# Kernel optimization log

Hardware: AMD Instinct MI355X
Metric: run time of the kernel (lower is better)

Reference implementation:

```python
import jax, jax.numpy as jnp
import numpy as np

NH, NKV, HD = 16, 4, 64  # num_heads, num_kv_heads, head_dim
ROPE_BASE = 10000.0


def setup_inputs() -> dict:
    key = jax.random.key(0)
    ks = jax.random.split(key, 5)
    B, S, D = 2, 2048, 1024
    x = jax.random.normal(ks[0], (B, S, D), dtype=jnp.float32)
    # torch Linear layout: [out_features, in_features], xavier-ish scale
    Wq = jax.random.normal(ks[1], (NH * HD, D), dtype=jnp.float32) * 0.02
    Wk = jax.random.normal(ks[2], (NKV * HD, D), dtype=jnp.float32) * 0.02
    Wv = jax.random.normal(ks[3], (NKV * HD, D), dtype=jnp.float32) * 0.02
    Wo = jax.random.normal(ks[4], (D, NH * HD), dtype=jnp.float32) * 0.02
    return {"x": x, "Wq": Wq, "Wk": Wk, "Wv": Wv, "Wo": Wo}


def _rotate_half(t):
    t1, t2 = jnp.split(t, 2, axis=-1)
    return jnp.concatenate([-t2, t1], axis=-1)


def _rope_cos_sin(seq_len, dtype):
    inv_freq = 1.0 / (ROPE_BASE ** (jnp.arange(0, HD, 2, dtype=jnp.float32) / HD))
    freqs = jnp.outer(jnp.arange(seq_len, dtype=jnp.float32), inv_freq)  # [S, HD/2]
    emb = jnp.concatenate([freqs, freqs], axis=-1)                       # [S, HD]
    return jnp.cos(emb).astype(dtype), jnp.sin(emb).astype(dtype)


def reference(x, Wq, Wk, Wv, Wo):
    B, S, D = x.shape
    scale = 1.0 / np.sqrt(HD)
    # projections (torch Linear: y = x @ W.T)
    q = jnp.einsum('bsd,ed->bse', x, Wq).reshape(B, S, NH, HD).transpose(0, 2, 1, 3)
    k = jnp.einsum('bsd,ed->bse', x, Wk).reshape(B, S, NKV, HD).transpose(0, 2, 1, 3)
    v = jnp.einsum('bsd,ed->bse', x, Wv).reshape(B, S, NKV, HD).transpose(0, 2, 1, 3)
    # RoPE
    cos, sin = _rope_cos_sin(S, x.dtype)
    cos = cos[None, None]  # [1,1,S,HD]
    sin = sin[None, None]
    q = q * cos + _rotate_half(q) * sin
    k = k * cos + _rotate_half(k) * sin
    # GQA: repeat kv heads (matches expand+reshape: head h = kvh*rep + r)
    rep = NH // NKV
    k = jnp.repeat(k, rep, axis=1)  # [B,NH,S,HD]
    v = jnp.repeat(v, rep, axis=1)
    # scaled dot-product attention, causal
    scores = jnp.einsum('bhqd,bhkd->bhqk', q, k) * scale
    causal = jnp.triu(jnp.ones((S, S), dtype=bool), k=1)
    scores = jnp.where(causal, jnp.float32(-jnp.inf), scores)
    attn = jax.nn.softmax(scores.astype(jnp.float32), axis=-1).astype(q.dtype)
    out = jnp.einsum('bhqk,bhkd->bhqd', attn, v)
    out = out.transpose(0, 2, 1, 3).reshape(B, S, NH * HD)
    return jnp.einsum('bse,de->bsd', out, Wo)
```

## Files before the change

### kernel.cpp

```cpp
#include <hip/hip_runtime.h>
#include <hip/hip_bf16.h>
#include <math.h>

#define B_    2
#define S_    2048
#define D_    1024
#define NH_   16
#define NKV_  4
#define HD_   64
#define NTOK  (B_ * S_)
#define QKVN  (NH_ * HD_ + 2 * NKV_ * HD_)
#define REP   (NH_ / NKV_)

#define LOG2E 1.4426950408889634f

typedef __attribute__((ext_vector_type(8))) short short8;
typedef __attribute__((ext_vector_type(4))) float f32x4;

__device__ short  g_xb[(size_t)NTOK * D_];
__device__ short  g_wqkv[(size_t)QKVN * D_];
__device__ short  g_wob[(size_t)D_ * NH_ * HD_];
__device__ float  g_rc[(size_t)S_ * 32];
__device__ float  g_rs[(size_t)S_ * 32];
__device__ short  g_qb[(size_t)B_ * NH_  * S_ * HD_];
__device__ short  g_kb[(size_t)B_ * NKV_ * S_ * HD_];
__device__ short  g_vt[(size_t)B_ * NKV_ * HD_ * S_];
__device__ short  g_ao[(size_t)NTOK * NH_ * HD_];

static __device__ inline short f2bf(float f) {
  __hip_bfloat16 h = __float2bfloat16(f);
  return *reinterpret_cast<short*>(&h);
}
static __device__ inline unsigned pack2(float lo, float hi) {
  return ((unsigned)(unsigned short)f2bf(hi) << 16) | (unsigned)(unsigned short)f2bf(lo);
}

#define NX4   (NTOK * D_ / 4)
#define NWQ4  (NH_ * HD_ * D_ / 4)
#define NWK4  (NKV_ * HD_ * D_ / 4)
#define NWV4  NWK4
#define NWO4  (D_ * NH_ * HD_ / 4)
#define NCVT  (NX4 + NWQ4 + NWK4 + NWV4 + NWO4)

__global__ __launch_bounds__(256) void convert_all(const float* __restrict__ x,
                                                   const float* __restrict__ wq,
                                                   const float* __restrict__ wk,
                                                   const float* __restrict__ wv,
                                                   const float* __restrict__ wo) {
  int i = blockIdx.x * blockDim.x + threadIdx.x;
  if (i >= NCVT) return;
  const float* src; short* dst; int off;
  if (i < NX4)                          { src = x;  dst = g_xb;   off = i; }
  else if (i < NX4 + NWQ4)              { src = wq; dst = g_wqkv; off = i - NX4; }
  else if (i < NX4 + NWQ4 + NWK4)       { src = wk; dst = g_wqkv + (size_t)NWQ4 * 4;          off = i - NX4 - NWQ4; }
  else if (i < NX4 + NWQ4 + NWK4 + NWV4){ src = wv; dst = g_wqkv + (size_t)(NWQ4 + NWK4) * 4; off = i - NX4 - NWQ4 - NWK4; }
  else                                  { src = wo; dst = g_wob;  off = i - NX4 - NWQ4 - NWK4 - NWV4; }
  float4 v = ((const float4*)src)[off];
  short4 s;
  s.x = f2bf(v.x); s.y = f2bf(v.y); s.z = f2bf(v.z); s.w = f2bf(v.w);
  ((short4*)dst)[off] = s;
}

__global__ __launch_bounds__(256) void rope_tbl() {
  int i = blockIdx.x * blockDim.x + threadIdx.x;
  if (i >= S_ * 32) return;
  const int d = i & 31, s = i >> 5;
  const float inv = exp2f((float)d * (-13.287712379549449f / 32.0f));
  const float ang = (float)s * inv;
  float sn, cs;
  sincosf(ang, &sn, &cs);
  g_rc[i] = cs; g_rs[i] = sn;
}

__global__ __launch_bounds__(256) void gemm_qkv_rope() {
  const int w = threadIdx.x >> 6, lane = threadIdx.x & 63;
  const int m0 = blockIdx.x * 128 + w * 32;
  const int nb = blockIdx.y;
  const int n0 = nb * 64;
  const int lr = lane & 15, lk = (lane >> 4) * 8;

  f32x4 acc[2][4] = {};
  for (int k0 = 0; k0 < D_; k0 += 32) {
    short8 a0 = *(const short8*)(g_xb + (size_t)(m0 + lr) * D_ + k0 + lk);
    short8 a1 = *(const short8*)(g_xb + (size_t)(m0 + 16 + lr) * D_ + k0 + lk);
#pragma unroll
    for (int bj = 0; bj < 4; ++bj) {
      short8 bf = *(const short8*)(g_wqkv + (size_t)(n0 + bj * 16 + lr) * D_ + k0 + lk);
      acc[0][bj] = __builtin_amdgcn_mfma_f32_16x16x32_bf16(a0, bf, acc[0][bj], 0, 0, 0);
      acc[1][bj] = __builtin_amdgcn_mfma_f32_16x16x32_bf16(a1, bf, acc[1][bj], 0, 0, 0);
    }
  }
  const int rb = (lane >> 4) * 4;

  if (nb < 20) {
    const float sc = (nb < 16) ? 0.125f * LOG2E : 1.0f;
    short* const base = (nb < 16) ? g_qb : g_kb;
    const int hh = (nb < 16) ? nb : (nb - 16);
    const int nhh = (nb < 16) ? NH_ : NKV_;
#pragma unroll
    for (int af = 0; af < 2; ++af)
#pragma unroll
      for (int bj = 0; bj < 2; ++bj) {
        const int d0 = bj * 16 + lr;
#pragma unroll
        for (int r = 0; r < 4; ++r) {
          const int tok = m0 + af * 16 + rb + r;
          const int bI = tok >> 11, s = tok & (S_ - 1);
          const float c  = g_rc[s * 32 + d0];
          const float sn = g_rs[s * 32 + d0];
          const float lo = acc[af][bj][r], hi = acc[af][bj + 2][r];
          short* dp = base + (((size_t)(bI * nhh + hh)) * S_ + s) * HD_;
          dp[d0]      = f2bf((lo * c - hi * sn) * sc);
          dp[d0 + 32] = f2bf((hi * c + lo * sn) * sc);
        }
      }
  } else {
    const int kvh = nb - 20;
#pragma unroll
    for (int af = 0; af < 2; ++af)
#pragma unroll
      for (int bj = 0; bj < 4; ++bj) {
        const int d = bj * 16 + lr;
        const int tok0 = m0 + af * 16 + rb;
        const int bI = tok0 >> 11, s0 = tok0 & (S_ - 1);
        short4 s4;
        s4.x = f2bf(acc[af][bj][0]); s4.y = f2bf(acc[af][bj][1]);
        s4.z = f2bf(acc[af][bj][2]); s4.w = f2bf(acc[af][bj][3]);
        *(short4*)(g_vt + (((size_t)(bI * NKV_ + kvh)) * HD_ + d) * S_ + s0) = s4;
      }
  }
}

__global__ __launch_bounds__(256) void attn_mfma() {
  const int bh  = blockIdx.x;
  const int b   = bh >> 4, h = bh & 15;
  const int kvh = h >> 2;
  const int qw  = (int)(gridDim.y - 1 - blockIdx.y);
  const int w   = threadIdx.x >> 6;
  const int lane = threadIdx.x & 63;
  const int g = lane >> 4, l = lane & 15;
  const int q0 = qw * 16;
  const int q_glob = q0 + l;

  const short* Qb = g_qb + ((size_t)bh * S_ + q0) * HD_;
  const short* Kb = g_kb + ((size_t)(b * NKV_ + kvh)) * S_ * HD_;
  const short* Vt = g_vt + ((size_t)(b * NKV_ + kvh)) * HD_ * S_;

  short8 qf[2];
  qf[0] = *(const short8*)(Qb + l * HD_ + g * 8);
  qf[1] = *(const short8*)(Qb + l * HD_ + 32 + g * 8);

  f32x4 o[4] = {};
  float m_run = -1e30f, l_part = 0.0f;

  const int nt = (q0 >> 5) + 1;
  for (int t = w; t < nt; t += 4) {
    const short* Kt = Kb + (size_t)(t * 32) * HD_;
    short8 kf0 = *(const short8*)(Kt + l * HD_ + g * 8);
    short8 kf1 = *(const short8*)(Kt + (16 + l) * HD_ + g * 8);
    short8 kf2 = *(const short8*)(Kt + l * HD_ + 32 + g * 8);
    short8 kf3 = *(const short8*)(Kt + (16 + l) * HD_ + 32 + g * 8);
    short8 vf[4];
#pragma unroll
    for (int df = 0; df < 4; ++df)
      vf[df] = *(const short8*)(Vt + (size_t)(df * 16 + l) * S_ + t * 32 + g * 8);

    f32x4 st[2] = {};
    st[0] = __builtin_amdgcn_mfma_f32_16x16x32_bf16(kf0, qf[0], st[0], 0, 0, 0);
    st[1] = __builtin_amdgcn_mfma_f32_16x16x32_bf16(kf1, qf[0], st[1], 0, 0, 0);
    st[0] = __builtin_amdgcn_mfma_f32_16x16x32_bf16(kf2, qf[1], st[0], 0, 0, 0);
    st[1] = __builtin_amdgcn_mfma_f32_16x16x32_bf16(kf3, qf[1], st[1], 0, 0, 0);

    float sv[2][4];
    float mt = -1e30f;
#pragma unroll
    for (int mf = 0; mf < 2; ++mf)
#pragma unroll
      for (int r = 0; r < 4; ++r) {
        const int kv = t * 32 + mf * 16 + g * 4 + r;
        float s = st[mf][r];
        s = (kv > q_glob) ? -1e30f : s;
        sv[mf][r] = s;
        mt = fmaxf(mt, s);
      }
    if (__any(mt > m_run + 8.0f)) {
      float mr = mt;
      mr = fmaxf(mr, __shfl_xor(mr, 16, 64));
      mr = fmaxf(mr, __shfl_xor(mr, 32, 64));
      const float m_new = fmaxf(m_run, mr);
      const float alpha = exp2f(m_run - m_new);
      l_part *= alpha;
#pragma unroll
      for (int df = 0; df < 4; ++df)
#pragma unroll
        for (int r = 0; r < 4; ++r) o[df][r] *= alpha;
      m_run = m_new;
    }
    float p[2][4];
#pragma unroll
    for (int mf = 0; mf < 2; ++mf)
#pragma unroll
      for (int r = 0; r < 4; ++r) {
        const float pv = exp2f(sv[mf][r] - m_run);
        p[mf][r] = pv;
        l_part += pv;
      }
    unsigned u0 = pack2(p[0][0], p[0][1]);
    unsigned u1 = pack2(p[0][2], p[0][3]);
    unsigned u2 = pack2(p[1][0], p[1][1]);
    unsigned u3 = pack2(p[1][2], p[1][3]);
    const int srcA = ((g & 1) << 5) + l;
    const int srcB = srcA + 16;
    const unsigned a0 = __shfl(u0, srcA, 64), a2 = __shfl(u2, srcA, 64);
    const unsigned b1 = __shfl(u1, srcA, 64), b3 = __shfl(u3, srcA, 64);
    const unsigned c0 = __shfl(u0, srcB, 64), c2 = __shfl(u2, srcB, 64);
    const unsigned d1 = __shfl(u1, srcB, 64), d3 = __shfl(u3, srcB, 64);
    const bool hi = (g & 2);
    unsigned W[4];
    W[0] = hi ? a2 : a0;  W[1] = hi ? b3 : b1;
    W[2] = hi ? c2 : c0;  W[3] = hi ? d3 : d1;
    short8 pt = *reinterpret_cast<short8*>(W);

#pragma unroll
    for (int df = 0; df < 4; ++df)
      o[df] = __builtin_amdgcn_mfma_f32_16x16x32_bf16(vf[df], pt, o[df], 0, 0, 0);
  }

  float l1 = l_part + __shfl_xor(l_part, 16, 64);
  const float l_tot = l1 + __shfl_xor(l1, 32, 64);

  __shared__ float lds_m[4][16];
  __shared__ float lds_l[4][16];
  __shared__ float lds_o[4][16][68];
  if (g == 0) { lds_m[w][l] = m_run; lds_l[w][l] = l_tot; }
#pragma unroll
  for (int df = 0; df < 4; ++df)
#pragma unroll
    for (int r = 0; r < 4; ++r)
      lds_o[w][l][df * 16 + g * 4 + r] = o[df][r];
  __syncthreads();

  const int tid = threadIdx.x;
  const int q = tid & 15, dg = tid >> 4;
  float ms = lds_m[0][q];
#pragma unroll
  for (int w2 = 1; w2 < 4; ++w2) ms = fmaxf(ms, lds_m[w2][q]);
  float lsum = 0.0f;
  float od[4] = {0.0f, 0.0f, 0.0f, 0.0f};
#pragma unroll
  for (int w2 = 0; w2 < 4; ++w2) {
    const float sc = exp2f(lds_m[w2][q] - ms);
    lsum += lds_l[w2][q] * sc;
#pragma unroll
    for (int j = 0; j < 4; ++j) od[j] += sc * lds_o[w2][q][dg * 4 + j];
  }
  const float inv_l = 1.0f / lsum;
  short* optr = g_ao + ((size_t)(b * S_ + q0 + q)) * (NH_ * HD_) + h * HD_;
  short4 s4;
  s4.x = f2bf(od[0] * inv_l);
  s4.y = f2bf(od[1] * inv_l);
  s4.z = f2bf(od[2] * inv_l);
  s4.w = f2bf(od[3] * inv_l);
  *(short4*)(optr + dg * 4) = s4;
}

__global__ __launch_bounds__(256) void gemm_out(float* __restrict__ out) {
  const int w = threadIdx.x >> 6, lane = threadIdx.x & 63;
  const int m0 = blockIdx.x * 128 + w * 32;
  const int n0 = blockIdx.y * 64;
  const int lr = lane & 15, lk = (lane >> 4) * 8;
  const int K = NH_ * HD_;

  f32x4 acc[2][4] = {};
  for (int k0 = 0; k0 < K; k0 += 32) {
    short8 a0 = *(const short8*)(g_ao + (size_t)(m0 + lr) * K + k0 + lk);
    short8 a1 = *(const short8*)(g_ao + (size_t)(m0 + 16 + lr) * K + k0 + lk);
#pragma unroll
    for (int bj = 0; bj < 4; ++bj) {
      short8 bf = *(const short8*)(g_wob + (size_t)(n0 + bj * 16 + lr) * K + k0 + lk);
      acc[0][bj] = __builtin_amdgcn_mfma_f32_16x16x32_bf16(a0, bf, acc[0][bj], 0, 0, 0);
      acc[1][bj] = __builtin_amdgcn_mfma_f32_16x16x32_bf16(a1, bf, acc[1][bj], 0, 0, 0);
    }
  }
  const int rb = (lane >> 4) * 4;
#pragma unroll
  for (int af = 0; af < 2; ++af)
#pragma unroll
    for (int bj = 0; bj < 4; ++bj)
#pragma unroll
      for (int r = 0; r < 4; ++r)
        out[(size_t)(m0 + af * 16 + rb + r) * D_ + n0 + bj * 16 + lr] =
            acc[af][bj][r];
}

extern "C" void kernel_launch(void* const* d_in, const int* in_sizes, int n_in,
                              void* d_out, int out_size, void* d_ws, size_t ws_size,
                              hipStream_t stream) {
  const float* x  = (const float*)d_in[0];
  const float* Wq = (const float*)d_in[1];
  const float* Wk = (const float*)d_in[2];
  const float* Wv = (const float*)d_in[3];
  const float* Wo = (const float*)d_in[4];
  float* out = (float*)d_out;

  convert_all<<<(NCVT + 255) / 256, 256, 0, stream>>>(x, Wq, Wk, Wv, Wo);
  rope_tbl<<<(S_ * 32 + 255) / 256, 256, 0, stream>>>();
  {
    dim3 g(NTOK / 128, QKVN / 64);
    gemm_qkv_rope<<<g, 256, 0, stream>>>();
  }
  {
    dim3 g(B_ * NH_, S_ / 16);
    attn_mfma<<<g, 256, 0, stream>>>();
  }
  {
    dim3 g(NTOK / 128, D_ / 64);
    gemm_out<<<g, 256, 0, stream>>>(out);
  }
}
```

Before: 322.9 us.

## Pre-swizzle V into MFMA fragment layout and drop P-transpose shuffles

The QKV projection now writes V in a per-tile, per-lane fragment layout, so the attention kernel loads each V fragment with one contiguous short4 per lane. The PV product switches from 16x16x32 MFMAs, which required cross-lane shuffles to transpose P, to 16x16x16 MFMAs that consume the score accumulator layout directly. P is packed to bf16 with the hardware v_cvt_pk_bf16_f32 instruction. This removes eight shuffles and the selects per tile at the cost of twice as many, smaller PV MFMAs.

Measured after the change: 295.4 us. 1.09x faster.

```diff
diff --git a/kernel.cpp b/kernel.cpp
--- a/kernel.cpp
+++ b/kernel.cpp
@@ -15,7 +15,14 @@
 #define LOG2E 1.4426950408889634f
 
 typedef __attribute__((ext_vector_type(8))) short short8;
+typedef __attribute__((ext_vector_type(4))) short short4v;
 typedef __attribute__((ext_vector_type(4))) float f32x4;
+
+#if __has_builtin(__builtin_amdgcn_mfma_f32_16x16x16bf16_1k)
+#define MFMA16(acc, a, b) acc = __builtin_amdgcn_mfma_f32_16x16x16bf16_1k(a, b, acc, 0, 0, 0)
+#else
+#define MFMA16(acc, a, b) asm("v_mfma_f32_16x16x16_bf16 %0, %1, %2, %0" : "+v"(acc) : "v"(a), "v"(b))
+#endif
 
 __device__ short  g_xb[(size_t)NTOK * D_];
 __device__ short  g_wqkv[(size_t)QKVN * D_];
@@ -24,15 +31,12 @@
 __device__ float  g_rs[(size_t)S_ * 32];
 __device__ short  g_qb[(size_t)B_ * NH_  * S_ * HD_];
 __device__ short  g_kb[(size_t)B_ * NKV_ * S_ * HD_];
-__device__ short  g_vt[(size_t)B_ * NKV_ * HD_ * S_];
+__device__ short  g_vts[(size_t)B_ * NKV_ * HD_ * S_];
 __device__ short  g_ao[(size_t)NTOK * NH_ * HD_];
 
 static __device__ inline short f2bf(float f) {
   __hip_bfloat16 h = __float2bfloat16(f);
   return *reinterpret_cast<short*>(&h);
-}
-static __device__ inline unsigned pack2(float lo, float hi) {
-  return ((unsigned)(unsigned short)f2bf(hi) << 16) | (unsigned)(unsigned short)f2bf(lo);
 }
 
 #define NX4   (NTOK * D_ / 4)
@@ -120,13 +124,15 @@
     for (int af = 0; af < 2; ++af)
 #pragma unroll
       for (int bj = 0; bj < 4; ++bj) {
-        const int d = bj * 16 + lr;
         const int tok0 = m0 + af * 16 + rb;
-        const int bI = tok0 >> 11, s0 = tok0 & (S_ - 1);
+        const int bI = tok0 >> 11, sl = tok0 & (S_ - 1);
+        const int t = sl >> 5;
+        const int half = (sl >> 4) & 1;
         short4 s4;
         s4.x = f2bf(acc[af][bj][0]); s4.y = f2bf(acc[af][bj][1]);
         s4.z = f2bf(acc[af][bj][2]); s4.w = f2bf(acc[af][bj][3]);
-        *(short4*)(g_vt + (((size_t)(bI * NKV_ + kvh)) * HD_ + d) * S_ + s0) = s4;
+        *(short4*)(g_vts + ((((size_t)(bI * NKV_ + kvh) * 64 + t) * 2 + half) * 4 + bj) * 256
+                         + lane * 4) = s4;
       }
   }
 }
@@ -142,9 +148,9 @@
   const int q0 = qw * 16;
   const int q_glob = q0 + l;
 
-  const short* Qb = g_qb + ((size_t)bh * S_ + q0) * HD_;
-  const short* Kb = g_kb + ((size_t)(b * NKV_ + kvh)) * S_ * HD_;
-  const short* Vt = g_vt + ((size_t)(b * NKV_ + kvh)) * HD_ * S_;
+  const short* Qb  = g_qb + ((size_t)bh * S_ + q0) * HD_;
+  const short* Kb  = g_kb + ((size_t)(b * NKV_ + kvh)) * S_ * HD_;
+  const short* Vts = g_vts + (size_t)(b * NKV_ + kvh) * 64 * 2048 + lane * 4;
 
   short8 qf[2];
   qf[0] = *(const short8*)(Qb + l * HD_ + g * 8);
@@ -160,10 +166,13 @@
     short8 kf1 = *(const short8*)(Kt + (16 + l) * HD_ + g * 8);
     short8 kf2 = *(const short8*)(Kt + l * HD_ + 32 + g * 8);
     short8 kf3 = *(const short8*)(Kt + (16 + l) * HD_ + 32 + g * 8);
-    short8 vf[4];
-#pragma unroll
-    for (int df = 0; df < 4; ++df)
-      vf[df] = *(const short8*)(Vt + (size_t)(df * 16 + l) * S_ + t * 32 + g * 8);
+    const short* Vb = Vts + (size_t)t * 2048;
+    short4v vfrag[2][4];
+#pragma unroll
+    for (int mf = 0; mf < 2; ++mf)
+#pragma unroll
+      for (int df = 0; df < 4; ++df)
+        vfrag[mf][df] = *(const short4v*)(Vb + (mf * 4 + df) * 256);
 
     f32x4 st[2] = {};
     st[0] = __builtin_amdgcn_mfma_f32_16x16x32_bf16(kf0, qf[0], st[0], 0, 0, 0);
@@ -196,34 +205,22 @@
         for (int r = 0; r < 4; ++r) o[df][r] *= alpha;
       m_run = m_new;
     }
-    float p[2][4];
-#pragma unroll
-    for (int mf = 0; mf < 2; ++mf)
-#pragma unroll
-      for (int r = 0; r < 4; ++r) {
-        const float pv = exp2f(sv[mf][r] - m_run);
-        p[mf][r] = pv;
-        l_part += pv;
-      }
-    unsigned u0 = pack2(p[0][0], p[0][1]);
-    unsigned u1 = pack2(p[0][2], p[0][3]);
-    unsigned u2 = pack2(p[1][0], p[1][1]);
-    unsigned u3 = pack2(p[1][2], p[1][3]);
-    const int srcA = ((g & 1) << 5) + l;
-    const int srcB = srcA + 16;
-    const unsigned a0 = __shfl(u0, srcA, 64), a2 = __shfl(u2, srcA, 64);
-    const unsigned b1 = __shfl(u1, srcA, 64), b3 = __shfl(u3, srcA, 64);
-    const unsigned c0 = __shfl(u0, srcB, 64), c2 = __shfl(u2, srcB, 64);
-    const unsigned d1 = __shfl(u1, srcB, 64), d3 = __shfl(u3, srcB, 64);
-    const bool hi = (g & 2);
-    unsigned W[4];
-    W[0] = hi ? a2 : a0;  W[1] = hi ? b3 : b1;
-    W[2] = hi ? c2 : c0;  W[3] = hi ? d3 : d1;
-    short8 pt = *reinterpret_cast<short8*>(W);
-
-#pragma unroll
-    for (int df = 0; df < 4; ++df)
-      o[df] = __builtin_amdgcn_mfma_f32_16x16x32_bf16(vf[df], pt, o[df], 0, 0, 0);
+#pragma unroll
+    for (int mf = 0; mf < 2; ++mf) {
+      float p0 = exp2f(sv[mf][0] - m_run);
+      float p1 = exp2f(sv[mf][1] - m_run);
+      float p2 = exp2f(sv[mf][2] - m_run);
+      float p3 = exp2f(sv[mf][3] - m_run);
+      l_part += (p0 + p1) + (p2 + p3);
+      unsigned ulo, uhi;
+      asm("v_cvt_pk_bf16_f32 %0, %1, %2" : "=v"(ulo) : "v"(p0), "v"(p1));
+      asm("v_cvt_pk_bf16_f32 %0, %1, %2" : "=v"(uhi) : "v"(p2), "v"(p3));
+      unsigned pw[2] = {ulo, uhi};
+      short4v pf = *reinterpret_cast<const short4v*>(pw);
+#pragma unroll
+      for (int df = 0; df < 4; ++df)
+        MFMA16(o[df], vfrag[mf][df], pf);
+    }
   }
 
   float l1 = l_part + __shfl_xor(l_part, 16, 64);
```
